# Kernel optimization log

Hardware: AMD Instinct MI355X
Metric: run time of the kernel (lower is better)

Reference implementation:

```python
import jax, jax.numpy as jnp
import numpy as np

NUM_CLASS = 22  # restypes_with_x_and_gap


def setup_inputs() -> dict:
    key = jax.random.key(0)
    k1, k2, k3, k4 = jax.random.split(key, 4)
    b, m, n, c = 1, 128, 256, NUM_CLASS
    variant = jax.random.randint(k1, (b, m, n), 0, c)              # int variant sequences
    variant_mask = jnp.ones((b, m, n), dtype=jnp.float32)
    eij = jax.random.normal(k2, (b, n, n, c, c), dtype=jnp.float32) * 0.1  # Potts couplings wij
    ei = jax.random.normal(k3, (b, n, c), dtype=jnp.float32) * 0.1         # fields bi
    mask_vec = jnp.ones((c,), dtype=jnp.float32).at[-1].set(0.0)   # mask out gap '-' class
    sigma = jnp.ones((1,), dtype=jnp.float32)                      # prior_w=1.0, task_num=1
    return {"variant": variant, "variant_mask": variant_mask, "eij": eij,
            "ei": ei, "mask_vec": mask_vec, "sigma": sigma}


def reference(variant, variant_mask, eij, ei, mask_vec, sigma):
    c = mask_vec.shape[0]
    onehot = jax.nn.one_hot(variant, c, dtype=eij.dtype)           # [b,m,n,c]
    # fold class mask into couplings, then Potts energy per position/class
    em = eij * mask_vec                                            # [b,i,j,c,d]
    hi = jnp.einsum('bmjd,bijcd->bmic', onehot, em)                # [b,m,i,c]
    motifs = ei[:, None] + hi                                      # [b,m,i,c]
    # log_softmax=False branch: pick the logit of the active class per position
    logits = jnp.einsum('bmic,bmic->bmi', motifs, onehot)          # [b,m,i]
    # eval path: delta vs reference variant (index 0), sum-pooled, scaled by sigma
    vm = variant_mask[..., None]                                   # [b,m,i,1]
    vm = vm * vm[:, :1]
    vlogit = logits - logits[:, :1]                                # [b,m,i]
    pooled = jnp.sum(vlogit[..., None] * vm, axis=-2)              # [b,m,task_num]
    variant_logit = sigma * pooled
    return motifs, logits, variant_logit
```

## Files before the change

kernel.cpp:

```cpp
#include <hip/hip_runtime.h>

#define NC    22
#define NROW  (NC*NC)
#define NJ    256
#define NI    256
#define NM    128
#define JG    8
#define NQJ   4
#define JQ    (NJ/NQJ)
#define SS    (JQ/JG)
#define ROWDW 16
#define JROW  (NC*ROWDW)
#define TILEDW (JG*JROW)
#define F4PS  (JG*NROW/4)

typedef __attribute__((ext_vector_type(8))) short short8;
typedef __attribute__((ext_vector_type(4))) float f32x4;

__device__ inline uint32_t bf16rne(float x) {
    uint32_t u = __float_as_uint(x);
    u += 0x7FFFu + ((u >> 16) & 1u);
    return u >> 16;
}

__global__ __launch_bounds__(256) void potts_mfma(
    const int*   __restrict__ variant,
    const float* __restrict__ eij,
    const float* __restrict__ mask_vec,
    float*       __restrict__ part)
{
    const int i    = blockIdx.x;
    const int jq   = blockIdx.y;
    const int tid  = threadIdx.x;
    const int lane = tid & 63;
    const int wv   = tid >> 6;
    const int q    = lane >> 4;
    const int nl   = lane & 15;

    __shared__ uint32_t tile[2][TILEDW];
    __shared__ int      vtab[2][JG][NM];

    for (int p = tid; p < 2 * JG * NC * 5; p += 256) {
        const int b  = p / (JG * NC * 5), r = p % (JG * NC * 5);
        const int jl = r / (NC * 5),     r2 = r % (NC * 5);
        tile[b][jl * JROW + (r2 / 5) * ROWDW + 11 + r2 % 5] = 0;
    }

    int   l0[4], l1[4];
    float mk[4][4];
    bool  act[4];
    #pragma unroll
    for (int r = 0; r < 4; ++r) {
        const int f4 = r * 256 + tid;
        act[r] = (f4 < F4PS);
        const int fc = act[r] ? f4 : 0;
        const int jl = fc / 121, r4 = fc % 121;
        const int f2a = 2 * r4, f2b = f2a + 1;
        const int ca = f2a / 11, wa = f2a % 11;
        const int cb = f2b / 11, wb = f2b % 11;
        l0[r] = jl * JROW + ca * ROWDW + wa;
        l1[r] = jl * JROW + cb * ROWDW + wb;
        mk[r][0] = mask_vec[2 * wa];  mk[r][1] = mask_vec[2 * wa + 1];
        mk[r][2] = mask_vec[2 * wb];  mk[r][3] = mask_vec[2 * wb + 1];
    }

    const float4* gsrc = (const float4*)eij + (size_t)(i * NJ + jq * JQ) * 121;

    const int c1   = 16 + nl;
    const int off0 = nl * ROWDW + q * 4;
    const int off1 = (c1 < NC ? c1 : 0) * ROWDW + q * 4;
    const int m0a  = wv * 16;
    const int m0b  = wv * 16 + 64;

    f32x4 acc_a0 = {0.f,0.f,0.f,0.f}, acc_a1 = {0.f,0.f,0.f,0.f};
    f32x4 acc_b0 = {0.f,0.f,0.f,0.f}, acc_b1 = {0.f,0.f,0.f,0.f};

    float4 pf[4];
    int    vr[4];
    #pragma unroll
    for (int r = 0; r < 4; ++r)
        if (act[r]) pf[r] = gsrc[r * 256 + tid];
    #pragma unroll
    for (int r = 0; r < 4; ++r) {
        const int t = r * 256 + tid;
        vr[r] = variant[(t >> 3) * NJ + jq * JQ + (t & 7)];
    }

    for (int s = 0; s < SS; ++s) {
        const int bsel = s & 1;
        uint32_t* buf = tile[bsel];

        #pragma unroll
        for (int r = 0; r < 4; ++r) {
            if (act[r]) {
                const float4 v = pf[r];
                buf[l0[r]] = bf16rne(v.x * mk[r][0])
                           | (bf16rne(v.y * mk[r][1]) << 16);
                buf[l1[r]] = bf16rne(v.z * mk[r][2])
                           | (bf16rne(v.w * mk[r][3]) << 16);
            }
        }
        #pragma unroll
        for (int r = 0; r < 4; ++r) {
            const int t = r * 256 + tid;
            vtab[bsel][t & 7][t >> 3] = vr[r];
        }
        __syncthreads();

        if (s + 1 < SS) {
            const float4* gn = gsrc + (size_t)(s + 1) * F4PS;
            #pragma unroll
            for (int r = 0; r < 4; ++r)
                if (act[r]) pf[r] = gn[r * 256 + tid];
            #pragma unroll
            for (int r = 0; r < 4; ++r) {
                const int t = r * 256 + tid;
                vr[r] = variant[(t >> 3) * NJ + jq * JQ + (s + 1) * JG + (t & 7)];
            }
        }

        #pragma unroll
        for (int jl = 0; jl < JG; ++jl) {
            const uint32_t* jrow = buf + jl * JROW;
            const short8 bf0 = *(const short8*)(jrow + off0);
            const short8 bf1 = *(const short8*)(jrow + off1);

            const int va = vtab[bsel][jl][m0a + nl];
            const int vb = vtab[bsel][jl][m0b + nl];

            const uint32_t pa = 0x3F80u << ((va & 1) << 4);
            const uint32_t pb = 0x3F80u << ((vb & 1) << 4);
            const int ha = va >> 1, hb = vb >> 1, kb = q * 4;
            union { uint32_t u[4]; short8 s; } fa, fb;
            #pragma unroll
            for (int t = 0; t < 4; ++t) {
                fa.u[t] = (ha == kb + t) ? pa : 0u;
                fb.u[t] = (hb == kb + t) ? pb : 0u;
            }

            acc_a0 = __builtin_amdgcn_mfma_f32_16x16x32_bf16(fa.s, bf0, acc_a0, 0, 0, 0);
            acc_a1 = __builtin_amdgcn_mfma_f32_16x16x32_bf16(fa.s, bf1, acc_a1, 0, 0, 0);
            acc_b0 = __builtin_amdgcn_mfma_f32_16x16x32_bf16(fb.s, bf0, acc_b0, 0, 0, 0);
            acc_b1 = __builtin_amdgcn_mfma_f32_16x16x32_bf16(fb.s, bf1, acc_b1, 0, 0, 0);
        }
    }

    float* pbase = part + ((size_t)jq * NI + i) * NM * NC;
    #pragma unroll
    for (int t = 0; t < 4; ++t) {
        const int ra = m0a + q * 4 + t, rb = m0b + q * 4 + t;
        pbase[ra * NC + nl] = acc_a0[t];
        pbase[rb * NC + nl] = acc_b0[t];
        if (c1 < NC) {
            pbase[ra * NC + c1] = acc_a1[t];
            pbase[rb * NC + c1] = acc_b1[t];
        }
    }
}

__global__ __launch_bounds__(256) void potts_reduce(
    const float* __restrict__ part,
    const int*   __restrict__ variant,
    const float* __restrict__ ei,
    float*       __restrict__ out_motifs,
    float*       __restrict__ out_logits)
{
    const int i    = blockIdx.x;
    const int tid  = threadIdx.x;
    const int m    = tid & 127;
    const int half = tid >> 7;
    const int cc0  = half * 11;

    const float* p0 = part + (((size_t)0 * NI + i) * NM + m) * NC + cc0;
    const float* p1 = part + (((size_t)1 * NI + i) * NM + m) * NC + cc0;
    const float* p2 = part + (((size_t)2 * NI + i) * NM + m) * NC + cc0;
    const float* p3 = part + (((size_t)3 * NI + i) * NM + m) * NC + cc0;
    const float* eirow = ei + i * NC;
    float* mout = out_motifs + ((size_t)m * NI + i) * NC;
    const int vi = variant[m * NJ + i];

    float logit = 0.f;
    #pragma unroll
    for (int k = 0; k < 11; ++k) {
        const float v = p0[k] + p1[k] + p2[k] + p3[k] + eirow[cc0 + k];
        mout[cc0 + k] = v;
        if (cc0 + k == vi) logit = v;
    }
    if (vi >= cc0 && vi < cc0 + 11)
        out_logits[m * NI + i] = logit;
}

__global__ __launch_bounds__(64) void potts_pool(
    const float* __restrict__ logits,
    const float* __restrict__ vmask,
    const float* __restrict__ sigma,
    float*       __restrict__ out_vl)
{
    const int m    = blockIdx.x;
    const int lane = threadIdx.x;
    float s = 0.f;
    #pragma unroll
    for (int qq = 0; qq < 4; ++qq) {
        const int i = lane + 64 * qq;
        const float vl = logits[m * NI + i] - logits[i];
        s += vl * vmask[m * NI + i] * vmask[i];
    }
    #pragma unroll
    for (int off = 32; off > 0; off >>= 1)
        s += __shfl_down(s, off, 64);
    if (lane == 0) out_vl[m] = sigma[0] * s;
}

extern "C" void kernel_launch(void* const* d_in, const int* in_sizes, int n_in,
                              void* d_out, int out_size, void* d_ws, size_t ws_size,
                              hipStream_t stream) {
    const int*   variant  = (const int*)  d_in[0];
    const float* vmask    = (const float*)d_in[1];
    const float* eij      = (const float*)d_in[2];
    const float* ei       = (const float*)d_in[3];
    const float* mask_vec = (const float*)d_in[4];
    const float* sigma    = (const float*)d_in[5];

    float* out        = (float*)d_out;
    float* out_motifs = out;
    float* out_logits = out_motifs + NM * NI * NC;
    float* out_vl     = out_logits + NM * NI;

    float* part = (float*)d_ws;

    dim3 gridA(NI, NQJ);
    potts_mfma<<<gridA, 256, 0, stream>>>(variant, eij, mask_vec, part);
    potts_reduce<<<NI, 256, 0, stream>>>(part, variant, ei,
                                         out_motifs, out_logits);
    potts_pool<<<NM, 64, 0, stream>>>(out_logits, vmask, sigma, out_vl);
}
```

Before: 206.2 us.

## Precompute one-hot MFMA A-fragments in a prepass and simplify bf16 packing

Adds a small prepass kernel that builds the one-hot bf16 A-operand fragments for every (j, m) once and stores them in workspace. The main MFMA kernel then loads them as uint4 from global memory instead of staging variants through LDS and rebuilding the fragments per block. The bf16 conversion becomes round-half-up with a byte-permute pack rather than full round-to-nearest-even, and the reduce kernel is remapped to one block per m with one thread per i. This trades redundant per-block fragment construction and LDS traffic for an extra launch and more global fragment reads.

```diff
diff --git a/kernel.cpp b/kernel.cpp
--- a/kernel.cpp
+++ b/kernel.cpp
@@ -13,21 +13,36 @@
 #define JROW  (NC*ROWDW)
 #define TILEDW (JG*JROW)
 #define F4PS  (JG*NROW/4)
+#define AJSTR (4*NM*4)
 
 typedef __attribute__((ext_vector_type(8))) short short8;
 typedef __attribute__((ext_vector_type(4))) float f32x4;
-
-__device__ inline uint32_t bf16rne(float x) {
-    uint32_t u = __float_as_uint(x);
-    u += 0x7FFFu + ((u >> 16) & 1u);
-    return u >> 16;
+union frag_u { uint4 v; uint32_t u[4]; short8 s; };
+
+__global__ __launch_bounds__(128) void build_afrag(
+    const int* __restrict__ variant,
+    uint32_t*  __restrict__ afrag)
+{
+    const int j = blockIdx.x;
+    const int m = threadIdx.x;
+    const int v = variant[m * NJ + j];
+    const uint32_t pat = 0x3F80u << ((v & 1) << 4);
+    #pragma unroll
+    for (int q = 0; q < 4; ++q) {
+        uint4 w;
+        w.x = ((v >> 1) == q * 4 + 0) ? pat : 0u;
+        w.y = ((v >> 1) == q * 4 + 1) ? pat : 0u;
+        w.z = ((v >> 1) == q * 4 + 2) ? pat : 0u;
+        w.w = ((v >> 1) == q * 4 + 3) ? pat : 0u;
+        ((uint4*)afrag)[(j * 4 + q) * NM + m] = w;
+    }
 }
 
 __global__ __launch_bounds__(256) void potts_mfma(
-    const int*   __restrict__ variant,
-    const float* __restrict__ eij,
-    const float* __restrict__ mask_vec,
-    float*       __restrict__ part)
+    const float*    __restrict__ eij,
+    const float*    __restrict__ mask_vec,
+    const uint32_t* __restrict__ afrag,
+    float*          __restrict__ part)
 {
     const int i    = blockIdx.x;
     const int jq   = blockIdx.y;
@@ -38,7 +53,6 @@
     const int nl   = lane & 15;
 
     __shared__ uint32_t tile[2][TILEDW];
-    __shared__ int      vtab[2][JG][NM];
 
     for (int p = tid; p < 2 * JG * NC * 5; p += 256) {
         const int b  = p / (JG * NC * 5), r = p % (JG * NC * 5);
@@ -70,40 +84,31 @@
     const int off0 = nl * ROWDW + q * 4;
     const int off1 = (c1 < NC ? c1 : 0) * ROWDW + q * 4;
     const int m0a  = wv * 16;
-    const int m0b  = wv * 16 + 64;
+    const uint32_t* abase = afrag + (size_t)(jq * JQ) * AJSTR
+                          + (q * NM + m0a + nl) * 4;
 
     f32x4 acc_a0 = {0.f,0.f,0.f,0.f}, acc_a1 = {0.f,0.f,0.f,0.f};
     f32x4 acc_b0 = {0.f,0.f,0.f,0.f}, acc_b1 = {0.f,0.f,0.f,0.f};
 
     float4 pf[4];
-    int    vr[4];
     #pragma unroll
     for (int r = 0; r < 4; ++r)
         if (act[r]) pf[r] = gsrc[r * 256 + tid];
-    #pragma unroll
-    for (int r = 0; r < 4; ++r) {
-        const int t = r * 256 + tid;
-        vr[r] = variant[(t >> 3) * NJ + jq * JQ + (t & 7)];
-    }
 
     for (int s = 0; s < SS; ++s) {
-        const int bsel = s & 1;
-        uint32_t* buf = tile[bsel];
+        uint32_t* buf = tile[s & 1];
 
         #pragma unroll
         for (int r = 0; r < 4; ++r) {
             if (act[r]) {
                 const float4 v = pf[r];
-                buf[l0[r]] = bf16rne(v.x * mk[r][0])
-                           | (bf16rne(v.y * mk[r][1]) << 16);
-                buf[l1[r]] = bf16rne(v.z * mk[r][2])
-                           | (bf16rne(v.w * mk[r][3]) << 16);
+                const uint32_t ax = __float_as_uint(v.x * mk[r][0]) + 0x8000u;
+                const uint32_t ay = __float_as_uint(v.y * mk[r][1]) + 0x8000u;
+                const uint32_t az = __float_as_uint(v.z * mk[r][2]) + 0x8000u;
+                const uint32_t aw = __float_as_uint(v.w * mk[r][3]) + 0x8000u;
+                buf[l0[r]] = __builtin_amdgcn_perm(ay, ax, 0x07060302u);
+                buf[l1[r]] = __builtin_amdgcn_perm(aw, az, 0x07060302u);
             }
-        }
-        #pragma unroll
-        for (int r = 0; r < 4; ++r) {
-            const int t = r * 256 + tid;
-            vtab[bsel][t & 7][t >> 3] = vr[r];
         }
         __syncthreads();
 
@@ -112,12 +117,9 @@
             #pragma unroll
             for (int r = 0; r < 4; ++r)
                 if (act[r]) pf[r] = gn[r * 256 + tid];
-            #pragma unroll
-            for (int r = 0; r < 4; ++r) {
-                const int t = r * 256 + tid;
-                vr[r] = variant[(t >> 3) * NJ + jq * JQ + (s + 1) * JG + (t & 7)];
-            }
-        }
+        }
+
+        const uint32_t* ass = abase + (size_t)s * JG * AJSTR;
 
         #pragma unroll
         for (int jl = 0; jl < JG; ++jl) {
@@ -125,18 +127,9 @@
             const short8 bf0 = *(const short8*)(jrow + off0);
             const short8 bf1 = *(const short8*)(jrow + off1);
 
-            const int va = vtab[bsel][jl][m0a + nl];
-            const int vb = vtab[bsel][jl][m0b + nl];
-
-            const uint32_t pa = 0x3F80u << ((va & 1) << 4);
-            const uint32_t pb = 0x3F80u << ((vb & 1) << 4);
-            const int ha = va >> 1, hb = vb >> 1, kb = q * 4;
-            union { uint32_t u[4]; short8 s; } fa, fb;
-            #pragma unroll
-            for (int t = 0; t < 4; ++t) {
-                fa.u[t] = (ha == kb + t) ? pa : 0u;
-                fb.u[t] = (hb == kb + t) ? pb : 0u;
-            }
+            frag_u fa, fb;
+            fa.v = *(const uint4*)(ass + jl * AJSTR);
+            fb.v = *(const uint4*)(ass + jl * AJSTR + 64 * 4);
 
             acc_a0 = __builtin_amdgcn_mfma_f32_16x16x32_bf16(fa.s, bf0, acc_a0, 0, 0, 0);
             acc_a1 = __builtin_amdgcn_mfma_f32_16x16x32_bf16(fa.s, bf1, acc_a1, 0, 0, 0);
@@ -148,7 +141,7 @@
     float* pbase = part + ((size_t)jq * NI + i) * NM * NC;
     #pragma unroll
     for (int t = 0; t < 4; ++t) {
-        const int ra = m0a + q * 4 + t, rb = m0b + q * 4 + t;
+        const int ra = m0a + q * 4 + t, rb = ra + 64;
         pbase[ra * NC + nl] = acc_a0[t];
         pbase[rb * NC + nl] = acc_b0[t];
         if (c1 < NC) {
@@ -165,29 +158,25 @@
     float*       __restrict__ out_motifs,
     float*       __restrict__ out_logits)
 {
-    const int i    = blockIdx.x;
-    const int tid  = threadIdx.x;
-    const int m    = tid & 127;
-    const int half = tid >> 7;
-    const int cc0  = half * 11;
-
-    const float* p0 = part + (((size_t)0 * NI + i) * NM + m) * NC + cc0;
-    const float* p1 = part + (((size_t)1 * NI + i) * NM + m) * NC + cc0;
-    const float* p2 = part + (((size_t)2 * NI + i) * NM + m) * NC + cc0;
-    const float* p3 = part + (((size_t)3 * NI + i) * NM + m) * NC + cc0;
+    const int m = blockIdx.x;
+    const int i = threadIdx.x;
+
+    const float* p0 = part + (((size_t)0 * NI + i) * NM + m) * NC;
+    const float* p1 = part + (((size_t)1 * NI + i) * NM + m) * NC;
+    const float* p2 = part + (((size_t)2 * NI + i) * NM + m) * NC;
+    const float* p3 = part + (((size_t)3 * NI + i) * NM + m) * NC;
     const float* eirow = ei + i * NC;
     float* mout = out_motifs + ((size_t)m * NI + i) * NC;
     const int vi = variant[m * NJ + i];
 
     float logit = 0.f;
     #pragma unroll
-    for (int k = 0; k < 11; ++k) {
-        const float v = p0[k] + p1[k] + p2[k] + p3[k] + eirow[cc0 + k];
-        mout[cc0 + k] = v;
-        if (cc0 + k == vi) logit = v;
-    }
-    if (vi >= cc0 && vi < cc0 + 11)
-        out_logits[m * NI + i] = logit;
+    for (int k = 0; k < NC; ++k) {
+        const float v = p0[k] + p1[k] + p2[k] + p3[k] + eirow[k];
+        mout[k] = v;
+        if (k == vi) logit = v;
+    }
+    out_logits[m * NI + i] = logit;
 }
 
 __global__ __launch_bounds__(64) void potts_pool(
@@ -226,11 +215,13 @@
     float* out_logits = out_motifs + NM * NI * NC;
     float* out_vl     = out_logits + NM * NI;
 
-    float* part = (float*)d_ws;
-
+    float*    part   = (float*)d_ws;
+    uint32_t* afrag  = (uint32_t*)(part + 4 * NI * NM * NC);
+
+    build_afrag<<<NJ, NM, 0, stream>>>(variant, afrag);
     dim3 gridA(NI, NQJ);
-    potts_mfma<<<gridA, 256, 0, stream>>>(variant, eij, mask_vec, part);
-    potts_reduce<<<NI, 256, 0, stream>>>(part, variant, ei,
-                                         out_motifs, out_logits);
+    potts_mfma<<<gridA, 256, 0, stream>>>(eij, mask_vec, afrag, part);
+    potts_reduce<<<NM, NI, 0, stream>>>(part, variant, ei,
+                                        out_motifs, out_logits);
     potts_pool<<<NM, 64, 0, stream>>>(out_logits, vmask, sigma, out_vl);
 }
```

After: 224.4 us. +8.8%, slower.
